# Performance work log

Hardware: AMD Instinct MI355X
Metric: run time of the kernel (lower is better)

## Reference

```python
import jax, jax.numpy as jnp
import numpy as np

E = 512
H = 8
HD = E // H
EPS = 1e-5


def setup_inputs() -> dict:
    key = jax.random.key(0)
    ks = jax.random.split(key, 12)
    S, B = 2048, 4
    bound_in = float(np.sqrt(6.0 / (3 * E + E)))  # xavier_uniform for in_proj
    inp = {
        "x": jax.random.normal(ks[0], (S, B, E), dtype=jnp.float32),
        "in_proj_weight": jax.random.uniform(ks[1], (3 * E, E), minval=-bound_in, maxval=bound_in, dtype=jnp.float32),
        "in_proj_bias": jnp.zeros((3 * E,), jnp.float32),
        "out_proj_weight": jax.random.normal(ks[2], (E, E), dtype=jnp.float32) * 0.02,
        "out_proj_bias": jnp.zeros((E,), jnp.float32),
        "ln1_gamma": jnp.ones((E,), jnp.float32),
        "ln1_beta": jnp.zeros((E,), jnp.float32),
        "fc1_weight": jax.random.normal(ks[3], (4 * E, E), dtype=jnp.float32) * 0.02,
        "fc1_bias": jnp.zeros((4 * E,), jnp.float32),
        "fc2_weight": jax.random.normal(ks[4], (E, 4 * E), dtype=jnp.float32) * 0.02,
        "fc2_bias": jnp.zeros((E,), jnp.float32),
        "ln2_gamma": jnp.ones((E,), jnp.float32),
        "ln2_beta": jnp.zeros((E,), jnp.float32),
    }
    return inp


def _layer_norm(x, gamma, beta):
    mu = jnp.mean(x, axis=-1, keepdims=True)
    var = jnp.mean(jnp.square(x - mu), axis=-1, keepdims=True)
    return (x - mu) * jax.lax.rsqrt(var + EPS) * gamma + beta


def _encoder_layer(x, in_w, in_b, out_w, out_b, g1, b1, fc1_w, fc1_b, fc2_w, fc2_b, g2, b2):
    S, B, _ = x.shape
    # --- self attention (hand-rolled, full S x S scores as in original) ---
    qkv = x @ in_w.T + in_b                      # [S, B, 3E]
    q, k, v = jnp.split(qkv, 3, axis=-1)         # each [S, B, E]
    # [S, B, E] -> [B*H, S, HD]
    def to_heads(t):
        return t.reshape(S, B * H, HD).transpose(1, 0, 2)
    q, k, v = to_heads(q), to_heads(k), to_heads(v)
    scores = jnp.einsum('bsd,btd->bst', q, k) / jnp.sqrt(jnp.float32(HD))  # [B*H, S, S]
    attn_w = jax.nn.softmax(scores, axis=-1)
    attn = jnp.einsum('bst,btd->bsd', attn_w, v)  # [B*H, S, HD]
    attn = attn.transpose(1, 0, 2).reshape(S, B, E)
    attn = attn @ out_w.T + out_b
    # --- residual + LN ---
    x = _layer_norm(x + attn, g1, b1)
    # --- FFN ---
    h = jax.nn.relu(x @ fc1_w.T + fc1_b)
    h = h @ fc2_w.T + fc2_b
    return _layer_norm(x + h, g2, b2)


def reference(x, in_proj_weight, in_proj_bias, out_proj_weight, out_proj_bias,
              ln1_gamma, ln1_beta, fc1_weight, fc1_bias, fc2_weight, fc2_bias,
              ln2_gamma, ln2_beta):
    return _encoder_layer(x, in_proj_weight, in_proj_bias, out_proj_weight, out_proj_bias,
                          ln1_gamma, ln1_beta, fc1_weight, fc1_bias, fc2_weight, fc2_bias,
                          ln2_gamma, ln2_beta)
```

## Files before the change

### kernel.cpp

```cpp
#include <hip/hip_runtime.h>

typedef _Float16 half8 __attribute__((ext_vector_type(8)));
typedef _Float16 half4 __attribute__((ext_vector_type(4)));
typedef float f32x4 __attribute__((ext_vector_type(4)));

static __device__ __forceinline__ f32x4 mfma16(half8 a, half8 b, f32x4 c) {
    return __builtin_amdgcn_mfma_f32_16x16x32_f16(a, b, c, 0, 0, 0);
}

static __device__ __forceinline__ void gload16(const void* g, const void* l) {
    __builtin_amdgcn_global_load_lds(
        (const __attribute__((address_space(1))) unsigned int*)(unsigned long long)g,
        (__attribute__((address_space(3))) unsigned int*)(unsigned int)(unsigned long long)l,
        16, 0, 0);
}

__global__ void __launch_bounds__(256) f32_to_f16(const float* __restrict__ in,
                                                  _Float16* __restrict__ out, int n) {
    long i = ((long)blockIdx.x * 256 + threadIdx.x) * 8;
    if (i >= n) return;
    f32x4 v0 = *(const f32x4*)(in + i);
    f32x4 v1 = *(const f32x4*)(in + i + 4);
    half8 h;
#pragma unroll
    for (int j = 0; j < 4; j++) { h[j] = (_Float16)v0[j]; h[4 + j] = (_Float16)v1[j]; }
    *(half8*)(out + i) = h;
}

template <int MODE, int NI>
__global__ void __launch_bounds__(256) gemm_bt(const _Float16* __restrict__ A,
                                               const _Float16* __restrict__ Bw,
                                               const float* __restrict__ bias,
                                               const float* __restrict__ resid,
                                               void* __restrict__ Cout,
                                               int M, int N, int K) {
    constexpr int BN = 32 * NI;
    __shared__ __align__(16) _Float16 As[2][128 * 32];
    __shared__ __align__(16) _Float16 Bs[2][BN * 32];
    const int tid = threadIdx.x;
    const int lane = tid & 63;
    const int w = tid >> 6;
    const int g = lane >> 4, l15 = lane & 15;
    const int wm = w >> 1, wn = w & 1;
    const long rowblk = (long)blockIdx.y * 128;
    const long colblk = (long)blockIdx.x * BN;

    const int lrow = lane >> 2;
    const int lcol = (lane & 3) * 8;

    f32x4 zero = {0.f, 0.f, 0.f, 0.f};
    f32x4 acc[4][NI];
#pragma unroll
    for (int i = 0; i < 4; i++)
#pragma unroll
        for (int j = 0; j < NI; j++) acc[i][j] = zero;

    auto stage = [&](int k0, int buf) {
        gload16(A + (rowblk + w * 32 + lrow) * (long)K + k0 + lcol, As[buf] + w * 1024);
        gload16(A + (rowblk + w * 32 + 16 + lrow) * (long)K + k0 + lcol, As[buf] + w * 1024 + 512);
#pragma unroll
        for (int c = 0; c < NI / 2; c++)
            gload16(Bw + (colblk + w * (8 * NI) + c * 16 + lrow) * (long)K + k0 + lcol,
                    Bs[buf] + w * (8 * NI) * 32 + c * 512);
    };

    stage(0, 0);
    __syncthreads();
    int buf = 0;
    for (int k0 = 0; k0 < K; k0 += 32) {
        if (k0 + 32 < K) stage(k0 + 32, buf ^ 1);
        half8 af[4], bf[NI];
#pragma unroll
        for (int mi = 0; mi < 4; mi++)
            af[mi] = *(const half8*)(As[buf] + (wm * 64 + mi * 16 + l15) * 32 + g * 8);
#pragma unroll
        for (int ni = 0; ni < NI; ni++)
            bf[ni] = *(const half8*)(Bs[buf] + (wn * (16 * NI) + ni * 16 + l15) * 32 + g * 8);
#pragma unroll
        for (int mi = 0; mi < 4; mi++)
#pragma unroll
            for (int ni = 0; ni < NI; ni++)
                acc[mi][ni] = mfma16(af[mi], bf[ni], acc[mi][ni]);
        __syncthreads();
        buf ^= 1;
    }

    const long crow0 = rowblk + wm * 64 + g * 4;
    const long ccol0 = colblk + wn * (16 * NI) + l15;
#pragma unroll
    for (int mi = 0; mi < 4; mi++) {
#pragma unroll
        for (int ni = 0; ni < NI; ni++) {
            const long cc = ccol0 + ni * 16;
            const float bv = bias[cc];
#pragma unroll
            for (int r = 0; r < 4; r++) {
                const long rr = crow0 + mi * 16 + r;
                float v = acc[mi][ni][r] + bv;
                if (MODE == 1) v = fmaxf(v, 0.f);
                if (MODE == 2) {
                    ((float*)Cout)[rr * N + cc] = v + resid[rr * N + cc];
                } else if (MODE == 3) {
                    const long sel = cc >> 9;
                    const int hh = (int)(cc >> 6) & 7;
                    const int dd = (int)cc & 63;
                    const int ss = (int)(rr >> 2), bb = (int)rr & 3;
                    ((_Float16*)Cout)[sel * (32L * 2048 * 64) +
                                      ((long)(bb * 8 + hh) * 2048 + ss) * 64 + dd] = (_Float16)v;
                } else {
                    ((_Float16*)Cout)[rr * N + cc] = (_Float16)v;
                }
            }
        }
    }
    (void)M;
}

__global__ void __launch_bounds__(256) transpose_v(const _Float16* __restrict__ Vh,
                                                   _Float16* __restrict__ Vt) {
    __shared__ _Float16 T[64][72];
    const int tid = threadIdx.x;
    const int bh = blockIdx.y;
    const int t0 = blockIdx.x * 64;
    const _Float16* src = Vh + ((long)bh * 2048 + t0) * 64;
    const int row = tid >> 2, col = (tid & 3) * 16;
    *(half8*)&T[row][col] = *(const half8*)(src + row * 64 + col);
    *(half8*)&T[row][col + 8] = *(const half8*)(src + row * 64 + col + 8);
    __syncthreads();
    const int d = tid >> 2, tc = (tid & 3) * 16;
    half8 a, b;
#pragma unroll
    for (int j = 0; j < 8; j++) { a[j] = T[tc + j][d]; b[j] = T[tc + 8 + j][d]; }
    _Float16* dst = Vt + ((long)bh * 64 + d) * 2048 + t0 + tc;
    *(half8*)dst = a;
    *(half8*)(dst + 8) = b;
}

__global__ void __launch_bounds__(256) attn_fwd(const _Float16* __restrict__ Qh,
                                                const _Float16* __restrict__ Kh,
                                                const _Float16* __restrict__ Vt,
                                                _Float16* __restrict__ out) {
    __shared__ __align__(16) _Float16 Klds[2][64 * 64];
    __shared__ __align__(16) _Float16 Vlds[2][64 * 64];
    __shared__ __align__(16) _Float16 Plds[4][32 * 72];
    const int tid = threadIdx.x;
    const int lane = tid & 63;
    const int w = tid >> 6;
    const int g = lane >> 4, l15 = lane & 15;
    const int bh = blockIdx.y;
    const int b = bh >> 3, h = bh & 7;
    const int s0 = blockIdx.x * 128 + w * 32;
    const _Float16* Qb = Qh + (long)bh * 2048 * 64;
    const _Float16* Kb = Kh + (long)bh * 2048 * 64;
    const _Float16* Vb = Vt + (long)bh * 64 * 2048;

    const int srow = lane >> 3;
    const int scolb = (lane & 7) * 16;

    half8 qb[2][2];
#pragma unroll
    for (int mi = 0; mi < 2; mi++)
#pragma unroll
        for (int ks = 0; ks < 2; ks++)
            qb[mi][ks] = *(const half8*)(Qb + (s0 + mi * 16 + l15) * 64 + ks * 32 + g * 8);

    f32x4 zero = {0.f, 0.f, 0.f, 0.f};
    f32x4 o[2][4];
    float mst[2], lst[2];
#pragma unroll
    for (int mi = 0; mi < 2; mi++) {
#pragma unroll
        for (int di = 0; di < 4; di++) o[mi][di] = zero;
        mst[mi] = -1e30f;
        lst[mi] = 0.f;
    }

    auto stage = [&](int t0, int buf) {
#pragma unroll
        for (int j = 0; j < 2; j++) {
            const int row = w * 16 + j * 8 + srow;
            const int src = scolb ^ ((row & 7) << 4);
            gload16(Kb + (long)(t0 + row) * 64 + (src >> 1),
                    Klds[buf] + (w * 16 + j * 8) * 64);
            gload16(Vb + (long)row * 2048 + t0 + (src >> 1),
                    Vlds[buf] + (w * 16 + j * 8) * 64);
        }
    };

    stage(0, 0);
    __syncthreads();
    int buf = 0;

    for (int t0 = 0; t0 < 2048; t0 += 64) {
        if (t0 + 64 < 2048) stage(t0 + 64, buf ^ 1);

        f32x4 st[4][2];
#pragma unroll
        for (int ni = 0; ni < 4; ni++) {
#pragma unroll
            for (int mi = 0; mi < 2; mi++) st[ni][mi] = zero;
#pragma unroll
            for (int ks = 0; ks < 2; ks++) {
                const int t = ni * 16 + l15;
                const int cb = (ks * 64 + g * 16) ^ ((t & 7) << 4);
                half8 ka = *(const half8*)((const char*)Klds[buf] + t * 128 + cb);
                st[ni][0] = mfma16(ka, qb[0][ks], st[ni][0]);
                st[ni][1] = mfma16(ka, qb[1][ks], st[ni][1]);
            }
        }

        float corrO[2][4];
#pragma unroll
        for (int mi = 0; mi < 2; mi++) {
            float mx = st[0][mi][0];
#pragma unroll
            for (int ni = 0; ni < 4; ni++)
#pragma unroll
                for (int r = 0; r < 4; r++) mx = fmaxf(mx, st[ni][mi][r]);
            mx = fmaxf(mx, __shfl_xor(mx, 16));
            mx = fmaxf(mx, __shfl_xor(mx, 32));
            const float mnew = fmaxf(mst[mi], mx);
            const float corr = __expf((mst[mi] - mnew) * 0.125f);
            mst[mi] = mnew;
            float rs = 0.f;
#pragma unroll
            for (int ni = 0; ni < 4; ni++) {
                half4 pv4;
#pragma unroll
                for (int r = 0; r < 4; r++) {
                    float pe = __expf((st[ni][mi][r] - mnew) * 0.125f);
                    rs += pe;
                    pv4[r] = (_Float16)pe;
                }
                *(half4*)(&Plds[w][(mi * 16 + l15) * 72 + ni * 16 + g * 4]) = pv4;
            }
            rs += __shfl_xor(rs, 16);
            rs += __shfl_xor(rs, 32);
            lst[mi] = lst[mi] * corr + rs;
#pragma unroll
            for (int r = 0; r < 4; r++) corrO[mi][r] = __shfl(corr, g * 4 + r);
        }

#pragma unroll
        for (int mi = 0; mi < 2; mi++)
#pragma unroll
            for (int di = 0; di < 4; di++)
#pragma unroll
                for (int r = 0; r < 4; r++) o[mi][di][r] *= corrO[mi][r];

        half8 pa[2][2];
#pragma unroll
        for (int mi = 0; mi < 2; mi++)
#pragma unroll
            for (int ks = 0; ks < 2; ks++)
                pa[mi][ks] = *(const half8*)(&Plds[w][(mi * 16 + l15) * 72 + ks * 32 + g * 8]);
#pragma unroll
        for (int di = 0; di < 4; di++)
#pragma unroll
            for (int ks = 0; ks < 2; ks++) {
                const int d = di * 16 + l15;
                const int cb = (ks * 64 + g * 16) ^ ((d & 7) << 4);
                half8 vb = *(const half8*)((const char*)Vlds[buf] + d * 128 + cb);
                o[0][di] = mfma16(pa[0][ks], vb, o[0][di]);
                o[1][di] = mfma16(pa[1][ks], vb, o[1][di]);
            }

        __syncthreads();
        buf ^= 1;
    }

#pragma unroll
    for (int mi = 0; mi < 2; mi++) {
#pragma unroll
        for (int r = 0; r < 4; r++) {
            const float lr = __shfl(lst[mi], g * 4 + r);
            const float inv = 1.f / lr;
            const long srowg = (long)((s0 + mi * 16 + g * 4 + r) * 4 + b) * 512;
#pragma unroll
            for (int di = 0; di < 4; di++)
                out[srowg + h * 64 + di * 16 + l15] = (_Float16)(o[mi][di][r] * inv);
        }
    }
}

__global__ void __launch_bounds__(256) ln_rows(const float* __restrict__ in,
                                               const float* __restrict__ gamma,
                                               const float* __restrict__ beta,
                                               float* __restrict__ outf,
                                               _Float16* __restrict__ outh) {
    const int tid = threadIdx.x, lane = tid & 63, w = tid >> 6;
    const long row = (long)blockIdx.x * 4 + w;
    const float* p = in + row * 512 + lane * 8;
    f32x4 v0 = *(const f32x4*)p;
    f32x4 v1 = *(const f32x4*)(p + 4);
    float s = v0[0] + v0[1] + v0[2] + v0[3] + v1[0] + v1[1] + v1[2] + v1[3];
    float q = v0[0] * v0[0] + v0[1] * v0[1] + v0[2] * v0[2] + v0[3] * v0[3] +
              v1[0] * v1[0] + v1[1] * v1[1] + v1[2] * v1[2] + v1[3] * v1[3];
#pragma unroll
    for (int off = 1; off < 64; off <<= 1) {
        s += __shfl_xor(s, off);
        q += __shfl_xor(q, off);
    }
    const float mu = s * (1.0f / 512.0f);
    const float var = q * (1.0f / 512.0f) - mu * mu;
    const float rstd = rsqrtf(var + 1e-5f);
    const float* gp = gamma + lane * 8;
    const float* bp = beta + lane * 8;
    f32x4 g0 = *(const f32x4*)gp, g1 = *(const f32x4*)(gp + 4);
    f32x4 b0 = *(const f32x4*)bp, b1 = *(const f32x4*)(bp + 4);
    f32x4 o0, o1;
#pragma unroll
    for (int j = 0; j < 4; j++) {
        o0[j] = (v0[j] - mu) * rstd * g0[j] + b0[j];
        o1[j] = (v1[j] - mu) * rstd * g1[j] + b1[j];
    }
    float* op = outf + row * 512 + lane * 8;
    *(f32x4*)op = o0;
    *(f32x4*)(op + 4) = o1;
    if (outh) {
        half8 hh;
#pragma unroll
        for (int j = 0; j < 4; j++) { hh[j] = (_Float16)o0[j]; hh[4 + j] = (_Float16)o1[j]; }
        *(half8*)(outh + row * 512 + lane * 8) = hh;
    }
}

extern "C" void kernel_launch(void* const* d_in, const int* in_sizes, int n_in,
                              void* d_out, int out_size, void* d_ws, size_t ws_size,
                              hipStream_t stream) {
    const float* x    = (const float*)d_in[0];
    const float* inw  = (const float*)d_in[1];
    const float* inb  = (const float*)d_in[2];
    const float* outw = (const float*)d_in[3];
    const float* outb = (const float*)d_in[4];
    const float* g1   = (const float*)d_in[5];
    const float* b1   = (const float*)d_in[6];
    const float* f1w  = (const float*)d_in[7];
    const float* f1b  = (const float*)d_in[8];
    const float* f2w  = (const float*)d_in[9];
    const float* f2b  = (const float*)d_in[10];
    const float* g2   = (const float*)d_in[11];
    const float* b2   = (const float*)d_in[12];

    char* ws = (char*)d_ws;
    const long MB = 1024 * 1024;
    _Float16* X16   = (_Float16*)(ws + 0);
    _Float16* HEADS = (_Float16*)(ws + 8 * MB);
    _Float16* H16   = (_Float16*)(ws + 0);
    _Float16* VT    = (_Float16*)(ws + 32 * MB);
    _Float16* ATT   = (_Float16*)(ws + 40 * MB);
    float*    PRE   = (float*)(ws + 48 * MB);
    float*    YF    = (float*)(ws + 64 * MB);
    _Float16* Y16   = (_Float16*)(ws + 80 * MB);
    _Float16* WIN   = (_Float16*)(ws + 88 * MB);
    _Float16* WOUT  = (_Float16*)(ws + 90 * MB);
    _Float16* WF1   = (_Float16*)(ws + 91 * MB);
    _Float16* WF2   = (_Float16*)(ws + 93 * MB);

    _Float16* Qh = HEADS;
    _Float16* Kh = HEADS + 32L * 2048 * 64;
    _Float16* Vh = HEADS + 2 * 32L * 2048 * 64;

    f32_to_f16<<<2048, 256, 0, stream>>>(x, X16, 8192 * 512);
    f32_to_f16<<<384, 256, 0, stream>>>(inw, WIN, 1536 * 512);
    f32_to_f16<<<128, 256, 0, stream>>>(outw, WOUT, 512 * 512);
    f32_to_f16<<<512, 256, 0, stream>>>(f1w, WF1, 2048 * 512);
    f32_to_f16<<<512, 256, 0, stream>>>(f2w, WF2, 512 * 2048);

    gemm_bt<3, 4><<<dim3(12, 64), 256, 0, stream>>>(X16, WIN, inb, nullptr, HEADS, 8192, 1536, 512);
    transpose_v<<<dim3(32, 32), 256, 0, stream>>>(Vh, VT);
    attn_fwd<<<dim3(16, 32), 256, 0, stream>>>(Qh, Kh, VT, ATT);
    gemm_bt<2, 2><<<dim3(8, 64), 256, 0, stream>>>(ATT, WOUT, outb, x, PRE, 8192, 512, 512);
    ln_rows<<<2048, 256, 0, stream>>>(PRE, g1, b1, YF, Y16);
    gemm_bt<1, 4><<<dim3(16, 64), 256, 0, stream>>>(Y16, WF1, f1b, nullptr, H16, 8192, 2048, 512);
    gemm_bt<2, 2><<<dim3(8, 64), 256, 0, stream>>>(H16, WF2, f2b, YF, PRE, 8192, 512, 2048);
    ln_rows<<<2048, 256, 0, stream>>>(PRE, g2, b2, (float*)d_out, nullptr);
}
```

Before: 319.4 us.

## Fold softmax scale into Q, transpose PV output, swizzle P LDS, set wave priority

Q is pre-scaled by log2(e)/sqrt(HD) in the QKV projection epilogue, so attention can use exp2 directly without a per-element multiply. The PV MFMA operands are swapped so the output accumulator is laid out transposed. This keeps per-lane row statistics aligned with the O columns, removing the corr/l shuffles, and lets the epilogue write half4 vectors. The P tile in LDS drops its padding in favour of an XOR swizzle, and s_setprio raises wave priority around the MFMA blocks to improve interleaving. Storing Q pre-scaled in fp16 slightly changes rounding.

```diff
diff --git a/kernel.cpp b/kernel.cpp
--- a/kernel.cpp
+++ b/kernel.cpp
@@ -105,6 +105,7 @@
                     const int hh = (int)(cc >> 6) & 7;
                     const int dd = (int)cc & 63;
                     const int ss = (int)(rr >> 2), bb = (int)rr & 3;
+                    if (sel == 0) v *= 0.18033688f;
                     ((_Float16*)Cout)[sel * (32L * 2048 * 64) +
                                       ((long)(bb * 8 + hh) * 2048 + ss) * 64 + dd] = (_Float16)v;
                 } else {
@@ -142,7 +143,7 @@
                                                 _Float16* __restrict__ out) {
     __shared__ __align__(16) _Float16 Klds[2][64 * 64];
     __shared__ __align__(16) _Float16 Vlds[2][64 * 64];
-    __shared__ __align__(16) _Float16 Plds[4][32 * 72];
+    __shared__ __align__(16) _Float16 Plds[4][32 * 64];
     const int tid = threadIdx.x;
     const int lane = tid & 63;
     const int w = tid >> 6;
@@ -165,12 +166,12 @@
             qb[mi][ks] = *(const half8*)(Qb + (s0 + mi * 16 + l15) * 64 + ks * 32 + g * 8);
 
     f32x4 zero = {0.f, 0.f, 0.f, 0.f};
-    f32x4 o[2][4];
+    f32x4 ot[2][4];
     float mst[2], lst[2];
 #pragma unroll
     for (int mi = 0; mi < 2; mi++) {
 #pragma unroll
-        for (int di = 0; di < 4; di++) o[mi][di] = zero;
+        for (int di = 0; di < 4; di++) ot[mi][di] = zero;
         mst[mi] = -1e30f;
         lst[mi] = 0.f;
     }
@@ -194,6 +195,7 @@
     for (int t0 = 0; t0 < 2048; t0 += 64) {
         if (t0 + 64 < 2048) stage(t0 + 64, buf ^ 1);
 
+        __builtin_amdgcn_s_setprio(1);
         f32x4 st[4][2];
 #pragma unroll
         for (int ni = 0; ni < 4; ni++) {
@@ -208,8 +210,9 @@
                 st[ni][1] = mfma16(ka, qb[1][ks], st[ni][1]);
             }
         }
-
-        float corrO[2][4];
+        __builtin_amdgcn_s_setprio(0);
+
+        char* const pw = (char*)Plds[w] + l15 * 128;
 #pragma unroll
         for (int mi = 0; mi < 2; mi++) {
             float mx = st[0][mi][0];
@@ -220,7 +223,7 @@
             mx = fmaxf(mx, __shfl_xor(mx, 16));
             mx = fmaxf(mx, __shfl_xor(mx, 32));
             const float mnew = fmaxf(mst[mi], mx);
-            const float corr = __expf((mst[mi] - mnew) * 0.125f);
+            const float corr = __builtin_exp2f(mst[mi] - mnew);
             mst[mi] = mnew;
             float rs = 0.f;
 #pragma unroll
@@ -228,32 +231,29 @@
                 half4 pv4;
 #pragma unroll
                 for (int r = 0; r < 4; r++) {
-                    float pe = __expf((st[ni][mi][r] - mnew) * 0.125f);
+                    const float pe = __builtin_exp2f(st[ni][mi][r] - mnew);
                     rs += pe;
                     pv4[r] = (_Float16)pe;
                 }
-                *(half4*)(&Plds[w][(mi * 16 + l15) * 72 + ni * 16 + g * 4]) = pv4;
+                *(half4*)(pw + mi * 2048 + ((ni * 32 + g * 8) ^ ((l15 & 7) << 4))) = pv4;
             }
             rs += __shfl_xor(rs, 16);
             rs += __shfl_xor(rs, 32);
             lst[mi] = lst[mi] * corr + rs;
 #pragma unroll
-            for (int r = 0; r < 4; r++) corrO[mi][r] = __shfl(corr, g * 4 + r);
-        }
-
+            for (int di = 0; di < 4; di++)
+#pragma unroll
+                for (int r = 0; r < 4; r++) ot[mi][di][r] *= corr;
+        }
+
+        half8 pa[2][2];
 #pragma unroll
         for (int mi = 0; mi < 2; mi++)
 #pragma unroll
-            for (int di = 0; di < 4; di++)
-#pragma unroll
-                for (int r = 0; r < 4; r++) o[mi][di][r] *= corrO[mi][r];
-
-        half8 pa[2][2];
-#pragma unroll
-        for (int mi = 0; mi < 2; mi++)
-#pragma unroll
             for (int ks = 0; ks < 2; ks++)
-                pa[mi][ks] = *(const half8*)(&Plds[w][(mi * 16 + l15) * 72 + ks * 32 + g * 8]);
+                pa[mi][ks] = *(const half8*)(pw + mi * 2048 +
+                                             ((ks * 64 + g * 16) ^ ((l15 & 7) << 4)));
+        __builtin_amdgcn_s_setprio(1);
 #pragma unroll
         for (int di = 0; di < 4; di++)
 #pragma unroll
@@ -261,9 +261,10 @@
                 const int d = di * 16 + l15;
                 const int cb = (ks * 64 + g * 16) ^ ((d & 7) << 4);
                 half8 vb = *(const half8*)((const char*)Vlds[buf] + d * 128 + cb);
-                o[0][di] = mfma16(pa[0][ks], vb, o[0][di]);
-                o[1][di] = mfma16(pa[1][ks], vb, o[1][di]);
+                ot[0][di] = mfma16(vb, pa[0][ks], ot[0][di]);
+                ot[1][di] = mfma16(vb, pa[1][ks], ot[1][di]);
             }
+        __builtin_amdgcn_s_setprio(0);
 
         __syncthreads();
         buf ^= 1;
@@ -271,14 +272,14 @@
 
 #pragma unroll
     for (int mi = 0; mi < 2; mi++) {
-#pragma unroll
-        for (int r = 0; r < 4; r++) {
-            const float lr = __shfl(lst[mi], g * 4 + r);
-            const float inv = 1.f / lr;
-            const long srowg = (long)((s0 + mi * 16 + g * 4 + r) * 4 + b) * 512;
-#pragma unroll
-            for (int di = 0; di < 4; di++)
-                out[srowg + h * 64 + di * 16 + l15] = (_Float16)(o[mi][di][r] * inv);
+        const float inv = 1.f / lst[mi];
+        const long q = s0 + mi * 16 + l15;
+#pragma unroll
+        for (int di = 0; di < 4; di++) {
+            half4 hv;
+#pragma unroll
+            for (int r = 0; r < 4; r++) hv[r] = (_Float16)(ot[mi][di][r] * inv);
+            *(half4*)(out + (q * 4 + b) * 512 + h * 64 + di * 16 + g * 4) = hv;
         }
     }
 }
```

New measurement: 315.6 us. Within noise of the previous version (-1.2%).
